# Kernel optimization log

Measured on AMD Instinct MI355X. Metric: run time of the kernel, lower is better.

## Reference

```python
import jax, jax.numpy as jnp
import numpy as np


def _vieta_pell_basis(x, degree):
    # Iterative recurrence: V0 = 2, V1 = x, Vn = x*V_{n-1} + V_{n-2}
    basis = [2.0 * jnp.ones_like(x), x]
    for _ in range(2, degree + 1):
        basis.append(x * basis[-1] + basis[-2])
    return jnp.stack(basis[: degree + 1], axis=-1)  # [b, i, d+1]


def setup_inputs() -> dict:
    key = jax.random.key(0)
    k1, k2 = jax.random.split(key)
    batch, input_dim, output_dim, degree = 4096, 1024, 1024, 8
    x = jax.random.normal(k1, (batch, input_dim), dtype=jnp.float32)
    std = 1.0 / (input_dim * (degree + 1))
    vp_coeffs = jax.random.normal(k2, (input_dim, output_dim, degree + 1), dtype=jnp.float32) * std
    return {"x": x, "vp_coeffs": vp_coeffs}


def reference(x, vp_coeffs):
    degree = vp_coeffs.shape[-1] - 1
    xt = jnp.tanh(x)  # [b, i]
    vp_basis = _vieta_pell_basis(xt, degree)  # [b, i, d+1]
    y = jnp.einsum("bid,iod->bo", vp_basis, vp_coeffs)
    return y
```

## Files before the change

kernel.cpp:

```cpp
#include <hip/hip_runtime.h>
#include <hip/hip_bf16.h>

typedef unsigned short u16;
typedef unsigned int   u32;
typedef unsigned long long u64;

#define BATCH 4096
#define IDIM  1024
#define ODIM  1024
#define NDEG  9
#define KA    8192
#define KAH   (KA / 2)

typedef __attribute__((ext_vector_type(8))) short short8_t;
typedef __attribute__((ext_vector_type(4))) float f32x4;

__device__ __forceinline__ u16 f2bf(float f) {
    union { float f; u32 u; } v; v.f = f;
    u32 r = v.u + 0x7FFFu + ((v.u >> 16) & 1u);
    return (u16)(r >> 16);
}
__device__ __forceinline__ u32 pack2bf(float lo, float hi) {
    return (u32)f2bf(lo) | ((u32)f2bf(hi) << 16);
}
__device__ __forceinline__ float bf2f(u16 h) {
    union { u32 u; float f; } v; v.u = (u32)h << 16; return v.f;
}

__device__ __forceinline__ void gl_lds16(const u16* g, u16* l) {
    __builtin_amdgcn_global_load_lds(
        (const __attribute__((address_space(1))) void*)g,
        (__attribute__((address_space(3))) void*)l,
        16, 0, 0);
}

#define PB_TI 128
#define PB_TO 8
#define PB_J  (PB_TO * NDEG)
#define PB_LS 132

#define NB_B   1024
#define NB_A   8192

__global__ void prep_kernel(const float* __restrict__ x,
                            const float* __restrict__ c,
                            u16* __restrict__ A, u16* __restrict__ Bt,
                            float* __restrict__ Pr) {
    __shared__ u16 lds[PB_J * PB_LS];
    const int bb  = blockIdx.x;
    const int tid = threadIdx.x;

    if (bb < NB_B) {
        const int i0 = (bb & 7) * PB_TI;
        const int o0 = (bb >> 3) * PB_TO;
        const float* src = c + (size_t)i0 * (ODIM * NDEG) + (size_t)o0 * NDEG;
#pragma unroll
        for (int t = 0; t < 36; ++t) {
            int f  = t * 256 + tid;
            int ii = f / PB_J;
            int j  = f - ii * PB_J;
            float v = src[(size_t)ii * (ODIM * NDEG) + j];
            lds[j * PB_LS + ii] = f2bf(v);
        }
        __syncthreads();

        {
            int o   = tid >> 5;
            int sub = tid & 31;
            const u16* row = lds + (o * NDEG) * PB_LS + sub * 4;
            float s = bf2f(row[0]) + bf2f(row[1]) + bf2f(row[2]) + bf2f(row[3]);
#pragma unroll
            for (int m = 16; m >= 1; m >>= 1)
                s += __shfl_xor(s, m, 64);
            if (sub == 0)
                Pr[(size_t)(bb & 7) * ODIM + o0 + o] = s;
        }

#pragma unroll
        for (int t = 0; t < 9; ++t) {
            int g   = t * 256 + tid;
            int j   = g >> 5;
            int ii4 = (g & 31) << 2;
            int o   = j / NDEG;
            int d   = j - o * NDEG;
            if (d != 0) {
                u64 v = *(const u64*)(lds + j * PB_LS + ii4);
                *(u64*)(Bt + (size_t)(o0 + o) * KA + (d - 1) * 1024 + i0 + ii4) = v;
            }
        }
    } else {
        int t  = (bb - NB_B) * 256 + tid;
        int b  = t >> 9;
        int i2 = (t & 511) << 1;
        float2 xv = ((const float2*)x)[t];
        float t0 = tanhf(xv.x), t1 = tanhf(xv.y);
        u32* dst = (u32*)(A + (size_t)b * KA + i2);
        float a0 = 2.0f, a1 = 2.0f;
        float b0 = t0,  b1 = t1;
        dst[0] = pack2bf(t0, t1);
#pragma unroll
        for (int d = 2; d < NDEG; ++d) {
            float n0 = t0 * b0 + a0;
            float n1 = t1 * b1 + a1;
            dst[(size_t)(d - 1) * 512] = pack2bf(n0, n1);
            a0 = b0; b0 = n0; a1 = b1; b1 = n1;
        }
    }
}

__global__ __launch_bounds__(256, 2)
void gemm_kernel(const u16* __restrict__ A, const u16* __restrict__ B,
                 float* __restrict__ P) {
    __shared__ __align__(16) u16 ldsA[128 * 64];
    __shared__ __align__(16) u16 ldsB[128 * 64];

    const int tid  = threadIdx.x;
    const int lane = tid & 63;
    const int wave = tid >> 6;
    const int quad = lane >> 4;
    const int l15  = lane & 15;
    const int wm   = wave & 1;
    const int wn   = wave >> 1;

    const int bid = blockIdx.x;
    const int xcd = bid & 7;
    const int loc = bid >> 3;
    const int z   = xcd >> 2;
    const int bm  = ((xcd & 3) << 3) | (loc >> 3);
    const int bn  = loc & 7;
    const int kStart = z * KAH;

    const u16* ga[4]; const u16* gb[4];
    u16* la[4]; u16* lb[4];
#pragma unroll
    for (int t = 0; t < 4; ++t) {
        int s  = t * 256 + tid;
        int r  = s >> 3;
        int sc = (s & 7) ^ (r & 7);
        ga[t] = A + (size_t)(bm * 128 + r) * KA + kStart + sc * 8;
        gb[t] = B + (size_t)(bn * 128 + r) * KA + kStart + sc * 8;
        la[t] = ldsA + s * 8;
        lb[t] = ldsB + s * 8;
    }

    f32x4 acc[4][4];
#pragma unroll
    for (int mt = 0; mt < 4; ++mt)
#pragma unroll
        for (int nt = 0; nt < 4; ++nt)
            acc[mt][nt] = (f32x4){0.f, 0.f, 0.f, 0.f};

    const int nIter = KAH / 64;
    for (int it = 0; it < nIter; ++it) {
#pragma unroll
        for (int t = 0; t < 4; ++t) gl_lds16(ga[t], la[t]);
#pragma unroll
        for (int t = 0; t < 4; ++t) gl_lds16(gb[t], lb[t]);
        __syncthreads();

#pragma unroll
        for (int kk = 0; kk < 2; ++kk) {
            short8_t af[4], bfg[4];
#pragma unroll
            for (int mt = 0; mt < 4; ++mt) {
                int row = wm * 64 + mt * 16 + l15;
                int pc  = (kk * 4 + quad) ^ (row & 7);
                af[mt] = *(const short8_t*)(ldsA + (row * 8 + pc) * 8);
            }
#pragma unroll
            for (int nt = 0; nt < 4; ++nt) {
                int row = wn * 64 + nt * 16 + l15;
                int pc  = (kk * 4 + quad) ^ (row & 7);
                bfg[nt] = *(const short8_t*)(ldsB + (row * 8 + pc) * 8);
            }
#pragma unroll
            for (int mt = 0; mt < 4; ++mt)
#pragma unroll
                for (int nt = 0; nt < 4; ++nt)
                    acc[mt][nt] = __builtin_amdgcn_mfma_f32_16x16x32_bf16(
                        af[mt], bfg[nt], acc[mt][nt], 0, 0, 0);
        }
        __syncthreads();

#pragma unroll
        for (int t = 0; t < 4; ++t) { ga[t] += 64; gb[t] += 64; }
    }

    float* C = P + (size_t)z * BATCH * ODIM;
#pragma unroll
    for (int mt = 0; mt < 4; ++mt) {
#pragma unroll
        for (int nt = 0; nt < 4; ++nt) {
            int row0 = bm * 128 + wm * 64 + mt * 16 + quad * 4;
            int col  = bn * 128 + wn * 64 + nt * 16 + l15;
#pragma unroll
            for (int r = 0; r < 4; ++r)
                C[(size_t)(row0 + r) * ODIM + col] = acc[mt][nt][r];
        }
    }
}

__global__ void reduce_kernel(const float* __restrict__ P,
                              const float* __restrict__ Pr,
                              float* __restrict__ out) {
    int t  = blockIdx.x * 256 + threadIdx.x;
    int o4 = t & 255;
    f32x4 a = ((const f32x4*)P)[t];
    a += ((const f32x4*)(P + (size_t)BATCH * ODIM))[t];
    f32x4 r = (f32x4){0.f, 0.f, 0.f, 0.f};
#pragma unroll
    for (int blk = 0; blk < 8; ++blk)
        r += ((const f32x4*)Pr)[blk * 256 + o4];
    ((f32x4*)out)[t] = a + r + r;
}

extern "C" void kernel_launch(void* const* d_in, const int* in_sizes, int n_in,
                              void* d_out, int out_size, void* d_ws, size_t ws_size,
                              hipStream_t stream) {
    const float* x      = (const float*)d_in[0];
    const float* coeffs = (const float*)d_in[1];
    float* out = (float*)d_out;

    u16*   A  = (u16*)d_ws;
    u16*   Bt = A + (size_t)BATCH * KA;
    float* Pr = (float*)(Bt + (size_t)ODIM * KA);
    float* P  = Pr + 8 * ODIM;

    prep_kernel<<<NB_B + NB_A, 256, 0, stream>>>(x, coeffs, A, Bt, Pr);
    gemm_kernel<<<512, 256, 0, stream>>>(A, Bt, P);
    reduce_kernel<<<BATCH * ODIM / 1024, 256, 0, stream>>>(P, Pr, out);
}
```

Baseline: 178.9 us.

## Rewrite GEMM with 256x256 tiles, double-buffered LDS prefetch, and 4-way split-K

The GEMM moves from 128x128 tiles with a single LDS buffer to 256x256 tiles using 8 waves and a double-buffered LDS pipeline. Global-to-LDS prefetches are interleaved between MFMA quarter-blocks using explicit waitcnt, barriers and setprio. Split-K grows from 2 to 4, with the first split written straight to the output and the reduce kernel summing the other three. The prep kernel now vectorises A-matrix generation to 8 elements per thread. The trade-off is more partial-sum traffic from the wider split-K and fragile hand-tuned synchronisation.

```diff
diff --git a/kernel.cpp b/kernel.cpp
--- a/kernel.cpp
+++ b/kernel.cpp
@@ -10,7 +10,10 @@
 #define ODIM  1024
 #define NDEG  9
 #define KA    8192
-#define KAH   (KA / 2)
+#define NZ    4
+#define KZ    (KA / NZ)
+#define GBK   64
+#define NT    (KZ / GBK)
 
 typedef __attribute__((ext_vector_type(8))) short short8_t;
 typedef __attribute__((ext_vector_type(4))) float f32x4;
@@ -34,13 +37,19 @@
         16, 0, 0);
 }
 
+#define BARRIER()   __builtin_amdgcn_s_barrier()
+#define WAIT_LGKM0() do { asm volatile("s_waitcnt lgkmcnt(0)" ::: "memory"); \
+                          __builtin_amdgcn_sched_barrier(0); } while (0)
+#define WAIT_VM8()  asm volatile("s_waitcnt vmcnt(8)" ::: "memory")
+#define WAIT_VM0()  asm volatile("s_waitcnt vmcnt(0)" ::: "memory")
+
 #define PB_TI 128
 #define PB_TO 8
 #define PB_J  (PB_TO * NDEG)
 #define PB_LS 132
 
 #define NB_B   1024
-#define NB_A   8192
+#define NB_A   2048
 
 __global__ void prep_kernel(const float* __restrict__ x,
                             const float* __restrict__ c,
@@ -90,114 +99,183 @@
         }
     } else {
         int t  = (bb - NB_B) * 256 + tid;
-        int b  = t >> 9;
-        int i2 = (t & 511) << 1;
-        float2 xv = ((const float2*)x)[t];
-        float t0 = tanhf(xv.x), t1 = tanhf(xv.y);
-        u32* dst = (u32*)(A + (size_t)b * KA + i2);
-        float a0 = 2.0f, a1 = 2.0f;
-        float b0 = t0,  b1 = t1;
-        dst[0] = pack2bf(t0, t1);
+        int b  = t >> 7;
+        int i8 = (t & 127) << 3;
+        const float4* xv = (const float4*)(x + ((size_t)t << 3));
+        float4 xa = xv[0], xb = xv[1];
+        float th[8] = {tanhf(xa.x), tanhf(xa.y), tanhf(xa.z), tanhf(xa.w),
+                       tanhf(xb.x), tanhf(xb.y), tanhf(xb.z), tanhf(xb.w)};
+        float va[8], vb[8];
+#pragma unroll
+        for (int j = 0; j < 8; ++j) { va[j] = 2.0f; vb[j] = th[j]; }
+        u16* dst = A + (size_t)b * KA + i8;
+        uint4 w;
+        w.x = pack2bf(th[0], th[1]); w.y = pack2bf(th[2], th[3]);
+        w.z = pack2bf(th[4], th[5]); w.w = pack2bf(th[6], th[7]);
+        *(uint4*)dst = w;
 #pragma unroll
         for (int d = 2; d < NDEG; ++d) {
-            float n0 = t0 * b0 + a0;
-            float n1 = t1 * b1 + a1;
-            dst[(size_t)(d - 1) * 512] = pack2bf(n0, n1);
-            a0 = b0; b0 = n0; a1 = b1; b1 = n1;
+            float nx[8];
+#pragma unroll
+            for (int j = 0; j < 8; ++j) {
+                nx[j] = th[j] * vb[j] + va[j];
+                va[j] = vb[j]; vb[j] = nx[j];
+            }
+            w.x = pack2bf(nx[0], nx[1]); w.y = pack2bf(nx[2], nx[3]);
+            w.z = pack2bf(nx[4], nx[5]); w.w = pack2bf(nx[6], nx[7]);
+            *(uint4*)(dst + (size_t)(d - 1) * 1024) = w;
         }
     }
 }
 
-__global__ __launch_bounds__(256, 2)
+#define MFMA_QUAD(MH, NH)                                                      \
+    __builtin_amdgcn_s_setprio(1);                                            \
+    _Pragma("unroll")                                                         \
+    for (int kk = 0; kk < 2; ++kk)                                            \
+        _Pragma("unroll")                                                     \
+        for (int m = 0; m < 4; ++m)                                           \
+            _Pragma("unroll")                                                 \
+            for (int n = 0; n < 2; ++n)                                       \
+                acc[(MH) * 4 + m][(NH) * 2 + n] =                             \
+                    __builtin_amdgcn_mfma_f32_16x16x32_bf16(                  \
+                        af[m][kk], bf[NH][n][kk],                             \
+                        acc[(MH) * 4 + m][(NH) * 2 + n], 0, 0, 0);            \
+    __builtin_amdgcn_s_setprio(0);
+
+__global__ __launch_bounds__(512, 2)
 void gemm_kernel(const u16* __restrict__ A, const u16* __restrict__ B,
-                 float* __restrict__ P) {
-    __shared__ __align__(16) u16 ldsA[128 * 64];
-    __shared__ __align__(16) u16 ldsB[128 * 64];
+                 float* __restrict__ P, float* __restrict__ out) {
+    __shared__ __align__(16) u16 ldsA[2][16384];
+    __shared__ __align__(16) u16 ldsB[2][16384];
 
     const int tid  = threadIdx.x;
     const int lane = tid & 63;
     const int wave = tid >> 6;
     const int quad = lane >> 4;
     const int l15  = lane & 15;
-    const int wm   = wave & 1;
-    const int wn   = wave >> 1;
+    const int wm   = wave >> 2;
+    const int wn   = wave & 3;
 
     const int bid = blockIdx.x;
-    const int xcd = bid & 7;
-    const int loc = bid >> 3;
-    const int z   = xcd >> 2;
-    const int bm  = ((xcd & 3) << 3) | (loc >> 3);
-    const int bn  = loc & 7;
-    const int kStart = z * KAH;
-
-    const u16* ga[4]; const u16* gb[4];
-    u16* la[4]; u16* lb[4];
-#pragma unroll
-    for (int t = 0; t < 4; ++t) {
-        int s  = t * 256 + tid;
+    const int z   = bid >> 6;
+    const int loc = bid & 63;
+    const int swz = (loc & 7) * 8 + (loc >> 3);
+    const int bm  = swz >> 2;
+    const int bn  = swz & 3;
+    const int kStart = z * KZ;
+
+    const u16* gA[4]; const u16* gB[4];
+#pragma unroll
+    for (int i = 0; i < 4; ++i) {
+        int s  = i * 512 + tid;
         int r  = s >> 3;
         int sc = (s & 7) ^ (r & 7);
-        ga[t] = A + (size_t)(bm * 128 + r) * KA + kStart + sc * 8;
-        gb[t] = B + (size_t)(bn * 128 + r) * KA + kStart + sc * 8;
-        la[t] = ldsA + s * 8;
-        lb[t] = ldsB + s * 8;
+        gA[i] = A + (size_t)(bm * 256 + r) * KA + kStart + sc * 8;
+        gB[i] = B + (size_t)(bn * 256 + r) * KA + kStart + sc * 8;
     }
 
-    f32x4 acc[4][4];
-#pragma unroll
-    for (int mt = 0; mt < 4; ++mt)
-#pragma unroll
-        for (int nt = 0; nt < 4; ++nt)
-            acc[mt][nt] = (f32x4){0.f, 0.f, 0.f, 0.f};
-
-    const int nIter = KAH / 64;
-    for (int it = 0; it < nIter; ++it) {
-#pragma unroll
-        for (int t = 0; t < 4; ++t) gl_lds16(ga[t], la[t]);
-#pragma unroll
-        for (int t = 0; t < 4; ++t) gl_lds16(gb[t], lb[t]);
-        __syncthreads();
-
-#pragma unroll
-        for (int kk = 0; kk < 2; ++kk) {
-            short8_t af[4], bfg[4];
-#pragma unroll
-            for (int mt = 0; mt < 4; ++mt) {
-                int row = wm * 64 + mt * 16 + l15;
-                int pc  = (kk * 4 + quad) ^ (row & 7);
-                af[mt] = *(const short8_t*)(ldsA + (row * 8 + pc) * 8);
+    f32x4 acc[8][4];
+#pragma unroll
+    for (int i = 0; i < 8; ++i)
+#pragma unroll
+        for (int j = 0; j < 4; ++j)
+            acc[i][j] = (f32x4){0.f, 0.f, 0.f, 0.f};
+
+#pragma unroll
+    for (int i = 0; i < 4; ++i) gl_lds16(gA[i], &ldsA[0][i * 4096 + tid * 8]);
+#pragma unroll
+    for (int i = 0; i < 4; ++i) gl_lds16(gB[i], &ldsB[0][i * 4096 + tid * 8]);
+#pragma unroll
+    for (int i = 0; i < 4; ++i) gl_lds16(gA[i] + GBK, &ldsA[1][i * 4096 + tid * 8]);
+#pragma unroll
+    for (int i = 0; i < 4; ++i) gl_lds16(gB[i] + GBK, &ldsB[1][i * 4096 + tid * 8]);
+#pragma unroll
+    for (int i = 0; i < 4; ++i) { gA[i] += 2 * GBK; gB[i] += 2 * GBK; }
+    WAIT_VM8();
+    BARRIER();
+
+    const int pc0  = quad ^ (l15 & 7);
+    const int pc1  = (4 + quad) ^ (l15 & 7);
+    const int offA = (wm * 128 + l15) * 64;
+    const int offB = (wn * 32 + l15) * 64;
+
+    short8_t af[4][2], bf[2][2][2];
+
+    for (int t = 0; t < NT; ++t) {
+        const u16* lA = ldsA[t & 1];
+        const u16* lB = ldsB[t & 1];
+        u16* sA = &ldsA[t & 1][tid * 8];
+        u16* sB = &ldsB[t & 1][tid * 8];
+        const bool pf = (t + 2 < NT);
+
+#pragma unroll
+        for (int m = 0; m < 4; ++m) {
+            af[m][0] = *(const short8_t*)(lA + offA + m * 1024 + pc0 * 8);
+            af[m][1] = *(const short8_t*)(lA + offA + m * 1024 + pc1 * 8);
+        }
+#pragma unroll
+        for (int nh = 0; nh < 2; ++nh)
+#pragma unroll
+            for (int n = 0; n < 2; ++n) {
+                bf[nh][n][0] = *(const short8_t*)(lB + offB + nh * 8192 + n * 1024 + pc0 * 8);
+                bf[nh][n][1] = *(const short8_t*)(lB + offB + nh * 8192 + n * 1024 + pc1 * 8);
             }
-#pragma unroll
-            for (int nt = 0; nt < 4; ++nt) {
-                int row = wn * 64 + nt * 16 + l15;
-                int pc  = (kk * 4 + quad) ^ (row & 7);
-                bfg[nt] = *(const short8_t*)(ldsB + (row * 8 + pc) * 8);
-            }
-#pragma unroll
-            for (int mt = 0; mt < 4; ++mt)
-#pragma unroll
-                for (int nt = 0; nt < 4; ++nt)
-                    acc[mt][nt] = __builtin_amdgcn_mfma_f32_16x16x32_bf16(
-                        af[mt], bfg[nt], acc[mt][nt], 0, 0, 0);
-        }
-        __syncthreads();
-
-#pragma unroll
-        for (int t = 0; t < 4; ++t) { ga[t] += 64; gb[t] += 64; }
+        BARRIER();
+        WAIT_LGKM0();
+        MFMA_QUAD(0, 0);
+        BARRIER();
+
+        if (pf) {
+            gl_lds16(gA[0], sA);
+            gl_lds16(gA[2], sA + 8192);
+            gl_lds16(gB[0], sB);
+            gl_lds16(gB[1], sB + 4096);
+            gl_lds16(gB[2], sB + 8192);
+            gl_lds16(gB[3], sB + 12288);
+        }
+        MFMA_QUAD(0, 1);
+        BARRIER();
+
+#pragma unroll
+        for (int m = 0; m < 4; ++m) {
+            af[m][0] = *(const short8_t*)(lA + offA + 4096 + m * 1024 + pc0 * 8);
+            af[m][1] = *(const short8_t*)(lA + offA + 4096 + m * 1024 + pc1 * 8);
+        }
+        BARRIER();
+        WAIT_LGKM0();
+        MFMA_QUAD(1, 1);
+        BARRIER();
+
+        if (pf) {
+            gl_lds16(gA[1], sA + 4096);
+            gl_lds16(gA[3], sA + 12288);
+        }
+        MFMA_QUAD(1, 0);
+        if (pf) {
+            WAIT_VM8();
+#pragma unroll
+            for (int i = 0; i < 4; ++i) { gA[i] += GBK; gB[i] += GBK; }
+        } else if (t + 1 < NT) {
+            WAIT_VM0();
+        }
+        BARRIER();
     }
 
-    float* C = P + (size_t)z * BATCH * ODIM;
-#pragma unroll
-    for (int mt = 0; mt < 4; ++mt) {
-#pragma unroll
-        for (int nt = 0; nt < 4; ++nt) {
-            int row0 = bm * 128 + wm * 64 + mt * 16 + quad * 4;
-            int col  = bn * 128 + wn * 64 + nt * 16 + l15;
-#pragma unroll
-            for (int r = 0; r < 4; ++r)
-                C[(size_t)(row0 + r) * ODIM + col] = acc[mt][nt][r];
-        }
-    }
+    float* C = (z == 0) ? out : P + (size_t)(z - 1) * (BATCH * ODIM);
+#pragma unroll
+    for (int mh = 0; mh < 2; ++mh)
+#pragma unroll
+        for (int m = 0; m < 4; ++m)
+#pragma unroll
+            for (int nh = 0; nh < 2; ++nh)
+#pragma unroll
+                for (int n = 0; n < 2; ++n) {
+                    int row0 = bm * 256 + wm * 128 + mh * 64 + m * 16 + quad * 4;
+                    int col  = bn * 256 + nh * 128 + wn * 32 + n * 16 + l15;
+#pragma unroll
+                    for (int r = 0; r < 4; ++r)
+                        C[(size_t)(row0 + r) * ODIM + col] = acc[mh * 4 + m][nh * 2 + n][r];
+                }
 }
 
 __global__ void reduce_kernel(const float* __restrict__ P,
@@ -205,8 +283,10 @@
                               float* __restrict__ out) {
     int t  = blockIdx.x * 256 + threadIdx.x;
     int o4 = t & 255;
-    f32x4 a = ((const f32x4*)P)[t];
+    f32x4 a = ((const f32x4*)out)[t];
+    a += ((const f32x4*)P)[t];
     a += ((const f32x4*)(P + (size_t)BATCH * ODIM))[t];
+    a += ((const f32x4*)(P + 2 * (size_t)BATCH * ODIM))[t];
     f32x4 r = (f32x4){0.f, 0.f, 0.f, 0.f};
 #pragma unroll
     for (int blk = 0; blk < 8; ++blk)
@@ -220,6 +300,7 @@
     const float* x      = (const float*)d_in[0];
     const float* coeffs = (const float*)d_in[1];
     float* out = (float*)d_out;
+    (void)ws_size;
 
     u16*   A  = (u16*)d_ws;
     u16*   Bt = A + (size_t)BATCH * KA;
@@ -227,6 +308,6 @@
     float* P  = Pr + 8 * ODIM;
 
     prep_kernel<<<NB_B + NB_A, 256, 0, stream>>>(x, coeffs, A, Bt, Pr);
-    gemm_kernel<<<512, 256, 0, stream>>>(A, Bt, P);
+    gemm_kernel<<<256, 512, 0, stream>>>(A, Bt, P, out);
     reduce_kernel<<<BATCH * ODIM / 1024, 256, 0, stream>>>(P, Pr, out);
 }
```

Result: slower. 188.6 us (+5.4%).
